# Kernel tuning notes

Measured on AMD Instinct MI355X. Metric: run time of the kernel, lower is better.

Reference implementation:

```python
import jax, jax.numpy as jnp
import numpy as np

NEG_POS_RATIO = 3

def hard_negative_mining(bg_loss, labels, neg_pos_ratio):
    # bg_loss: [B, P] = -log_softmax(conf)[..., 0]; labels: [B, P] int
    pos_mask = labels > 0                               # [B, P]
    num_pos = jnp.sum(pos_mask, axis=1, keepdims=True)  # [B, 1]
    num_neg = num_pos * neg_pos_ratio                   # [B, 1]
    # positives are excluded from the negative ranking
    masked = jnp.where(pos_mask, -jnp.inf, bg_loss)
    # rank of each prior when sorted by loss descending (0 = hardest negative)
    order = jnp.argsort(jnp.argsort(-masked, axis=1), axis=1)
    neg_mask = order < num_neg
    return pos_mask | neg_mask

def setup_inputs() -> dict:
    key = jax.random.key(0)
    k1, k2, k3, k4, k5 = jax.random.split(key, 5)
    B, P, C = 64, 8732, 81
    pred_loc = jax.random.normal(k1, (B, P, 4), dtype=jnp.float32)
    pred_conf = jax.random.normal(k2, (B, P, C), dtype=jnp.float32)
    gt_loc = jax.random.normal(k3, (B, P, 4), dtype=jnp.float32)
    raw_labels = jax.random.randint(k4, (B, P), 0, C)
    is_pos = jax.random.uniform(k5, (B, P)) < 0.02
    gt_labels = jnp.where(is_pos, raw_labels, 0).astype(jnp.int32)
    return {"pred_loc": pred_loc, "pred_conf": pred_conf, "gt_loc": gt_loc, "gt_labels": gt_labels}

def reference(pred_loc, pred_conf, gt_loc, gt_labels):
    # SSD MultiBox loss (training-mode forward of MultiBoxHeads)
    logp = jax.nn.log_softmax(pred_conf, axis=-1)           # [B, P, C]
    bg_loss = -logp[..., 0]                                 # [B, P]
    mask = jax.lax.stop_gradient(
        hard_negative_mining(jax.lax.stop_gradient(bg_loss), gt_labels, NEG_POS_RATIO))
    # cross-entropy with gt labels, summed over kept (pos + hard-neg) priors
    ce = -jnp.take_along_axis(logp, gt_labels[..., None].astype(jnp.int32), axis=-1)[..., 0]
    objectness_loss = jnp.sum(jnp.where(mask, ce, 0.0))
    # smooth L1 on positive priors only
    pos_mask = gt_labels > 0                                # [B, P]
    diff = pred_loc - gt_loc
    absd = jnp.abs(diff)
    sl1 = jnp.where(absd < 1.0, 0.5 * diff * diff, absd - 0.5)
    smooth_l1_loss = jnp.sum(jnp.where(pos_mask[..., None], sl1, 0.0))
    num_pos = jnp.maximum(jnp.sum(pos_mask), 1).astype(jnp.float32)
    return (objectness_loss / num_pos, smooth_l1_loss / num_pos)
```

## Files before the change

kernel.cpp:

```cpp
#include <hip/hip_runtime.h>
#include <cstdint>
#include <cstddef>

#define BATCH 64
#define PRI   8732
#define NCLS  81
#define NEGPOS 3
#define NTOT  (BATCH * PRI)
#define PPB   32
#define NWIN  (NTOT / PPB)
#define WFLOATS (PPB * NCLS)
#define WF4   (WFLOATS / 4)
#define NPERS 1792

__device__ __forceinline__ unsigned keymap(float f) {
    unsigned u = __float_as_uint(f);
    return (u & 0x80000000u) ? ~u : (u | 0x80000000u);
}

__device__ __forceinline__ void gl_lds16(const float4* g, float4* l) {
    __builtin_amdgcn_global_load_lds(
        (const __attribute__((address_space(1))) void*)(const void*)g,
        (__attribute__((address_space(3))) void*)(void*)l, 16, 0, 0);
}

__global__ __launch_bounds__(256) void k_lse(const float* __restrict__ conf,
                                             const int* __restrict__ labels,
                                             const float* __restrict__ ploc,
                                             const float* __restrict__ gloc,
                                             unsigned* __restrict__ keysg,
                                             float* __restrict__ cepart,
                                             float* __restrict__ slpart) {
    __shared__ float lds[2][WFLOATS];
    __shared__ int   labs[2][PPB];
    __shared__ float red0[4], red1[4];
    const int t = threadIdx.x;
    const int bid = blockIdx.x;

    float ceacc = 0.0f, slacc = 0.0f;

    auto stage = [&](int buf, int w) {
        const float4* g4 = reinterpret_cast<const float4*>(conf) + (size_t)w * WF4;
        float4* l4 = reinterpret_cast<float4*>(&lds[buf][0]);
        gl_lds16(&g4[t], &l4[t]);
        gl_lds16(&g4[t + 256], &l4[t + 256]);
        if (t < WF4 - 512) gl_lds16(&g4[t + 512], &l4[t + 512]);
        if (t < PPB) labs[buf][t] = labels[w * PPB + t];
    };

    stage(0, bid);
    __syncthreads();

    int cur = 0;
    for (int i = 0; ; ++i) {
        const int w  = bid + i * NPERS;
        const int wn = w + NPERS;
        const bool more = (wn < NWIN);
        if (more) stage(cur ^ 1, wn);

        const float* ldsw = &lds[cur][0];
        const int q   = t >> 3, h = t & 7;
        const int f0  = q * NCLS + 10 * h;
        const int len = (h == 7) ? 11 : 10;
        const int a0  = f0 & ~3;
        const int o   = f0 & 3;
        const int ve  = o + len;

        const float4* lp = reinterpret_cast<const float4*>(ldsw + a0);
        float4 v0 = lp[0], v1 = lp[1], v2 = lp[2], v3 = lp[3];
        v0.x = (o > 0) ? -INFINITY : v0.x;
        v0.y = (o > 1) ? -INFINITY : v0.y;
        v0.z = (o > 2) ? -INFINITY : v0.z;
        v2.z = (ve > 10) ? v2.z : -INFINITY;
        v2.w = (ve > 11) ? v2.w : -INFINITY;
        v3.x = (ve > 12) ? v3.x : -INFINITY;
        v3.y = (ve > 13) ? v3.y : -INFINITY;
        v3.z = -INFINITY;
        v3.w = -INFINITY;

        float m;
        {
            float a = fmaxf(fmaxf(v0.x, v0.y), fmaxf(v0.z, v0.w));
            float c = fmaxf(fmaxf(v1.x, v1.y), fmaxf(v1.z, v1.w));
            float d = fmaxf(fmaxf(v2.x, v2.y), fmaxf(v2.z, v2.w));
            float e = fmaxf(v3.x, v3.y);
            m = fmaxf(fmaxf(a, c), fmaxf(d, e));
        }
        float s =
            __expf(v0.x - m) + __expf(v0.y - m) + __expf(v0.z - m) + __expf(v0.w - m) +
            __expf(v1.x - m) + __expf(v1.y - m) + __expf(v1.z - m) + __expf(v1.w - m) +
            __expf(v2.x - m) + __expf(v2.y - m) + __expf(v2.z - m) + __expf(v2.w - m) +
            __expf(v3.x - m) + __expf(v3.y - m);

#pragma unroll
        for (int off = 1; off <= 4; off <<= 1) {
            const float mo = __shfl_xor(m, off, 64);
            const float so = __shfl_xor(s, off, 64);
            const float mn = fmaxf(m, mo);
            s = s * __expf(m - mn) + so * __expf(mo - mn);
            m = mn;
        }
        const float lse = m + __logf(s);

        if (h == 0) {
            const int p   = w * PPB + q;
            const int lab = labs[cur][q];
            const float c0 = ldsw[q * NCLS];
            unsigned key = 0u;
            if (lab > 0) {
                ceacc += lse - ldsw[q * NCLS + lab];
                const float4 pl = *reinterpret_cast<const float4*>(ploc + (size_t)p * 4);
                const float4 gl = *reinterpret_cast<const float4*>(gloc + (size_t)p * 4);
                float d, a;
                d = pl.x - gl.x; a = fabsf(d); slacc += (a < 1.0f) ? 0.5f * d * d : a - 0.5f;
                d = pl.y - gl.y; a = fabsf(d); slacc += (a < 1.0f) ? 0.5f * d * d : a - 0.5f;
                d = pl.z - gl.z; a = fabsf(d); slacc += (a < 1.0f) ? 0.5f * d * d : a - 0.5f;
                d = pl.w - gl.w; a = fabsf(d); slacc += (a < 1.0f) ? 0.5f * d * d : a - 0.5f;
            } else {
                key = keymap(lse - c0);
            }
            keysg[p] = key;
        }

        if (!more) break;
        __syncthreads();
        cur ^= 1;
    }

#pragma unroll
    for (int off = 32; off > 0; off >>= 1) {
        ceacc += __shfl_xor(ceacc, off, 64);
        slacc += __shfl_xor(slacc, off, 64);
    }
    const int wid = t >> 6, lane = t & 63;
    __syncthreads();
    if (lane == 0) { red0[wid] = ceacc; red1[wid] = slacc; }
    __syncthreads();
    if (t == 0) {
        cepart[bid] = red0[0] + red0[1] + red0[2] + red0[3];
        slpart[bid] = red1[0] + red1[1] + red1[2] + red1[3];
    }
}

__global__ __launch_bounds__(1024) void k_row(const unsigned* __restrict__ keysg,
                                              float* __restrict__ rowobj,
                                              float* __restrict__ rownp) {
    __shared__ unsigned keys_s[PRI];
    __shared__ unsigned hist[16][257];
    __shared__ unsigned ured[16];
    __shared__ float    fred[16];
    __shared__ unsigned sh_prefix, sh_r;
    __shared__ int      sh_flag;

    const int row  = blockIdx.x;
    const int tid  = threadIdx.x;
    const int wid  = tid >> 6;
    const int lane = tid & 63;
    const unsigned* krow = keysg + (size_t)row * PRI;

    unsigned np = 0;
    for (int j = tid; j < PRI; j += 1024) {
        const unsigned key = krow[j];
        keys_s[j] = key;
        np += (key == 0u) ? 1u : 0u;
    }
#pragma unroll
    for (int off = 32; off > 0; off >>= 1) np += __shfl_xor(np, off, 64);
    if (lane == 0) ured[wid] = np;
    __syncthreads();
    unsigned num_pos = 0;
#pragma unroll
    for (int w = 0; w < 16; ++w) num_pos += ured[w];
    const int k = (int)num_pos * NEGPOS;

    unsigned Kstar = 0xFFFFFFFFu;
    int r_eq = 0;
    bool take_all = false;
    if (k > 0) {
        unsigned prefix = 0;
        int r = k, flag = 0;
        unsigned* hist_flat = &hist[0][0];
        for (int level = 3; level >= 0; --level) {
            const int shift = level * 8;
            for (int i = tid; i < 16 * 257; i += 1024) hist_flat[i] = 0;
            __syncthreads();
            for (int j = tid; j < PRI; j += 1024) {
                const unsigned key = keys_s[j];
                if (key == 0u) continue;
                if (level < 3 && (key >> (shift + 8)) != (prefix >> (shift + 8))) continue;
                atomicAdd(&hist[wid][(key >> shift) & 255u], 1u);
            }
            __syncthreads();
            if (wid == 0) {
                const int b0 = lane * 4;
                unsigned h0 = 0, h1 = 0, h2 = 0, h3 = 0;
#pragma unroll
                for (int w = 0; w < 16; ++w) {
                    h0 += hist[w][b0]; h1 += hist[w][b0 + 1];
                    h2 += hist[w][b0 + 2]; h3 += hist[w][b0 + 3];
                }
                const unsigned loc = h0 + h1 + h2 + h3;
                unsigned ssum = loc;
#pragma unroll
                for (int o2 = 1; o2 < 64; o2 <<= 1) {
                    const unsigned t2 = __shfl_down(ssum, o2, 64);
                    if (lane + o2 < 64) ssum += t2;
                }
                const unsigned above = ssum - loc;
                const unsigned cum3 = above + h3;
                const unsigned cum2 = cum3 + h2;
                const unsigned cum1 = cum2 + h1;
                const unsigned cum0 = cum1 + h0;
                const unsigned long long msk = __ballot(cum0 >= (unsigned)r);
                if (msk == 0ULL) {
                    if (lane == 0) sh_flag = 1;
                } else {
                    const int L = 63 - __clzll(msk);
                    if (lane == L) {
                        unsigned selbin, cumsel, hsel;
                        if      (cum3 >= (unsigned)r) { selbin = b0 + 3; cumsel = cum3; hsel = h3; }
                        else if (cum2 >= (unsigned)r) { selbin = b0 + 2; cumsel = cum2; hsel = h2; }
                        else if (cum1 >= (unsigned)r) { selbin = b0 + 1; cumsel = cum1; hsel = h1; }
                        else                          { selbin = b0;     cumsel = cum0; hsel = h0; }
                        sh_prefix = prefix | (selbin << shift);
                        sh_r = (unsigned)r - (cumsel - hsel);
                        sh_flag = 0;
                    }
                }
            }
            __syncthreads();
            flag = sh_flag;
            if (flag) break;
            prefix = sh_prefix;
            r = (int)sh_r;
        }
        take_all = (flag != 0);
        if (!take_all) { Kstar = prefix; r_eq = r; }
    }

    float obj = 0.0f;
    if (k > 0) {
        for (int j = tid; j < PRI; j += 1024) {
            const unsigned key = keys_s[j];
            if (key != 0u && (take_all || key > Kstar))
                obj += __uint_as_float(key ^ 0x80000000u);
        }
        if (tid == 0 && !take_all)
            obj += (float)r_eq * __uint_as_float(Kstar ^ 0x80000000u);
    }

#pragma unroll
    for (int off = 32; off > 0; off >>= 1) obj += __shfl_xor(obj, off, 64);
    __syncthreads();
    if (lane == 0) fred[wid] = obj;
    __syncthreads();
    if (tid == 0) {
        float to = 0.0f;
#pragma unroll
        for (int w = 0; w < 16; ++w) to += fred[w];
        rowobj[row] = to;
        rownp[row]  = (float)num_pos;
    }
}

__global__ __launch_bounds__(256) void k_final(const float* __restrict__ cepart,
                                               const float* __restrict__ slpart,
                                               const float* __restrict__ rowobj,
                                               const float* __restrict__ rownp,
                                               float* __restrict__ out) {
    const int tid = threadIdx.x;
    float ce = 0.0f, sl = 0.0f;
    for (int i = tid; i < NPERS; i += 256) { ce += cepart[i]; sl += slpart[i]; }
    float ro = 0.0f, np = 0.0f;
    if (tid < BATCH) { ro = rowobj[tid]; np = rownp[tid]; }
#pragma unroll
    for (int off = 32; off > 0; off >>= 1) {
        ce += __shfl_xor(ce, off, 64);
        sl += __shfl_xor(sl, off, 64);
        ro += __shfl_xor(ro, off, 64);
        np += __shfl_xor(np, off, 64);
    }
    __shared__ float r0[4], r1[4], r2[4], r3[4];
    const int wid = tid >> 6, lane = tid & 63;
    if (lane == 0) { r0[wid] = ce; r1[wid] = sl; r2[wid] = ro; r3[wid] = np; }
    __syncthreads();
    if (tid == 0) {
        const float tce = r0[0] + r0[1] + r0[2] + r0[3];
        const float tsl = r1[0] + r1[1] + r1[2] + r1[3];
        const float tro = r2[0] + r2[1] + r2[2] + r2[3];
        const float tnp = r3[0] + r3[1] + r3[2] + r3[3];
        const float npos = fmaxf(tnp, 1.0f);
        out[0] = (tce + tro) / npos;
        out[1] = tsl / npos;
    }
}

extern "C" void kernel_launch(void* const* d_in, const int* in_sizes, int n_in,
                              void* d_out, int out_size, void* d_ws, size_t ws_size,
                              hipStream_t stream) {
    const float* pred_loc  = (const float*)d_in[0];
    const float* pred_conf = (const float*)d_in[1];
    const float* gt_loc    = (const float*)d_in[2];
    const int*   gt_labels = (const int*)d_in[3];
    float* out = (float*)d_out;

    unsigned* keysg   = (unsigned*)d_ws;
    float*    cepart  = (float*)(keysg + NTOT);
    float*    slpart  = cepart + NPERS;
    float*    rowobj  = slpart + NPERS;
    float*    rownp   = rowobj + BATCH;

    k_lse<<<NPERS, 256, 0, stream>>>(pred_conf, gt_labels, pred_loc, gt_loc,
                                     keysg, cepart, slpart);
    k_row<<<BATCH, 1024, 0, stream>>>(keysg, rowobj, rownp);
    k_final<<<1, 256, 0, stream>>>(cepart, slpart, rowobj, rownp, out);
}
```

Measured before the change: 59.35 us.

## Fuse LSE, row selection and final reduction into one persistent kernel

Merges the three kernels into one launch of 256 blocks of 1024 threads. Blocks first compute the log-sum-exp keys over 128-prior windows. The first 64 blocks then spin on a global atomic counter until every block has finished, run the per-row radix selection, and the last row block does the final reduction. This removes two kernel launches and their inter-kernel gaps. In exchange it adds a memset launch, relies on all 256 blocks being co-resident for the grid-wide spin wait, and cuts the number of blocks streaming the large conf tensor.

```diff
diff --git a/kernel.cpp b/kernel.cpp
--- a/kernel.cpp
+++ b/kernel.cpp
@@ -7,11 +7,11 @@
 #define NCLS  81
 #define NEGPOS 3
 #define NTOT  (BATCH * PRI)
-#define PPB   32
+#define PPB   128
 #define NWIN  (NTOT / PPB)
 #define WFLOATS (PPB * NCLS)
 #define WF4   (WFLOATS / 4)
-#define NPERS 1792
+#define NBLKM 256
 
 __device__ __forceinline__ unsigned keymap(float f) {
     unsigned u = __float_as_uint(f);
@@ -24,153 +24,177 @@
         (__attribute__((address_space(3))) void*)(void*)l, 16, 0, 0);
 }
 
-__global__ __launch_bounds__(256) void k_lse(const float* __restrict__ conf,
-                                             const int* __restrict__ labels,
-                                             const float* __restrict__ ploc,
-                                             const float* __restrict__ gloc,
-                                             unsigned* __restrict__ keysg,
-                                             float* __restrict__ cepart,
-                                             float* __restrict__ slpart) {
-    __shared__ float lds[2][WFLOATS];
-    __shared__ int   labs[2][PPB];
-    __shared__ float red0[4], red1[4];
+struct Phase1 {
+    float lds[2][WFLOATS];
+    int   labs[2][PPB];
+    float red0[16], red1[16];
+};
+struct Phase2 {
+    unsigned keys[PRI];
+    unsigned hist[16][257];
+    unsigned ured[16];
+    float    fred[16], fred2[16];
+    unsigned sh_prefix, sh_r;
+    int      sh_flag;
+};
+
+__global__ __launch_bounds__(1024) void k_all(const float* __restrict__ conf,
+                                              const int* __restrict__ labels,
+                                              const float* __restrict__ ploc,
+                                              const float* __restrict__ gloc,
+                                              unsigned* __restrict__ keysg,
+                                              float* __restrict__ cepart,
+                                              float* __restrict__ slpart,
+                                              unsigned* __restrict__ counter,
+                                              float* __restrict__ rowobj,
+                                              float* __restrict__ rownp,
+                                              float* __restrict__ out) {
+    __shared__ union { Phase1 p1; Phase2 p2; } sm;
     const int t = threadIdx.x;
     const int bid = blockIdx.x;
-
-    float ceacc = 0.0f, slacc = 0.0f;
-
-    auto stage = [&](int buf, int w) {
-        const float4* g4 = reinterpret_cast<const float4*>(conf) + (size_t)w * WF4;
-        float4* l4 = reinterpret_cast<float4*>(&lds[buf][0]);
-        gl_lds16(&g4[t], &l4[t]);
-        gl_lds16(&g4[t + 256], &l4[t + 256]);
-        if (t < WF4 - 512) gl_lds16(&g4[t + 512], &l4[t + 512]);
-        if (t < PPB) labs[buf][t] = labels[w * PPB + t];
-    };
-
-    stage(0, bid);
-    __syncthreads();
-
-    int cur = 0;
-    for (int i = 0; ; ++i) {
-        const int w  = bid + i * NPERS;
-        const int wn = w + NPERS;
-        const bool more = (wn < NWIN);
-        if (more) stage(cur ^ 1, wn);
-
-        const float* ldsw = &lds[cur][0];
-        const int q   = t >> 3, h = t & 7;
-        const int f0  = q * NCLS + 10 * h;
-        const int len = (h == 7) ? 11 : 10;
-        const int a0  = f0 & ~3;
-        const int o   = f0 & 3;
-        const int ve  = o + len;
-
-        const float4* lp = reinterpret_cast<const float4*>(ldsw + a0);
-        float4 v0 = lp[0], v1 = lp[1], v2 = lp[2], v3 = lp[3];
-        v0.x = (o > 0) ? -INFINITY : v0.x;
-        v0.y = (o > 1) ? -INFINITY : v0.y;
-        v0.z = (o > 2) ? -INFINITY : v0.z;
-        v2.z = (ve > 10) ? v2.z : -INFINITY;
-        v2.w = (ve > 11) ? v2.w : -INFINITY;
-        v3.x = (ve > 12) ? v3.x : -INFINITY;
-        v3.y = (ve > 13) ? v3.y : -INFINITY;
-        v3.z = -INFINITY;
-        v3.w = -INFINITY;
-
-        float m;
-        {
-            float a = fmaxf(fmaxf(v0.x, v0.y), fmaxf(v0.z, v0.w));
-            float c = fmaxf(fmaxf(v1.x, v1.y), fmaxf(v1.z, v1.w));
-            float d = fmaxf(fmaxf(v2.x, v2.y), fmaxf(v2.z, v2.w));
-            float e = fmaxf(v3.x, v3.y);
-            m = fmaxf(fmaxf(a, c), fmaxf(d, e));
-        }
-        float s =
-            __expf(v0.x - m) + __expf(v0.y - m) + __expf(v0.z - m) + __expf(v0.w - m) +
-            __expf(v1.x - m) + __expf(v1.y - m) + __expf(v1.z - m) + __expf(v1.w - m) +
-            __expf(v2.x - m) + __expf(v2.y - m) + __expf(v2.z - m) + __expf(v2.w - m) +
-            __expf(v3.x - m) + __expf(v3.y - m);
-
-#pragma unroll
-        for (int off = 1; off <= 4; off <<= 1) {
-            const float mo = __shfl_xor(m, off, 64);
-            const float so = __shfl_xor(s, off, 64);
-            const float mn = fmaxf(m, mo);
-            s = s * __expf(m - mn) + so * __expf(mo - mn);
-            m = mn;
-        }
-        const float lse = m + __logf(s);
-
-        if (h == 0) {
-            const int p   = w * PPB + q;
-            const int lab = labs[cur][q];
-            const float c0 = ldsw[q * NCLS];
-            unsigned key = 0u;
-            if (lab > 0) {
-                ceacc += lse - ldsw[q * NCLS + lab];
-                const float4 pl = *reinterpret_cast<const float4*>(ploc + (size_t)p * 4);
-                const float4 gl = *reinterpret_cast<const float4*>(gloc + (size_t)p * 4);
-                float d, a;
-                d = pl.x - gl.x; a = fabsf(d); slacc += (a < 1.0f) ? 0.5f * d * d : a - 0.5f;
-                d = pl.y - gl.y; a = fabsf(d); slacc += (a < 1.0f) ? 0.5f * d * d : a - 0.5f;
-                d = pl.z - gl.z; a = fabsf(d); slacc += (a < 1.0f) ? 0.5f * d * d : a - 0.5f;
-                d = pl.w - gl.w; a = fabsf(d); slacc += (a < 1.0f) ? 0.5f * d * d : a - 0.5f;
-            } else {
-                key = keymap(lse - c0);
-            }
-            keysg[p] = key;
-        }
-
-        if (!more) break;
+    const int wid = t >> 6, lane = t & 63;
+
+    {
+        float ceacc = 0.0f, slacc = 0.0f;
+        const float4* conf4 = reinterpret_cast<const float4*>(conf);
+
+        auto stage = [&](int buf, int w) {
+            const float4* g4 = conf4 + (size_t)w * WF4;
+            float4* l4 = reinterpret_cast<float4*>(&sm.p1.lds[buf][0]);
+            gl_lds16(&g4[t], &l4[t]);
+            gl_lds16(&g4[t + 1024], &l4[t + 1024]);
+            if (t < WF4 - 2048) gl_lds16(&g4[t + 2048], &l4[t + 2048]);
+            if (t < PPB) sm.p1.labs[buf][t] = labels[w * PPB + t];
+        };
+
+        stage(0, bid);
         __syncthreads();
-        cur ^= 1;
-    }
-
-#pragma unroll
-    for (int off = 32; off > 0; off >>= 1) {
-        ceacc += __shfl_xor(ceacc, off, 64);
-        slacc += __shfl_xor(slacc, off, 64);
-    }
-    const int wid = t >> 6, lane = t & 63;
-    __syncthreads();
-    if (lane == 0) { red0[wid] = ceacc; red1[wid] = slacc; }
+
+        int cur = 0;
+        for (int i = 0; ; ++i) {
+            const int w  = bid + i * NBLKM;
+            const int wn = w + NBLKM;
+            const bool more = (wn < NWIN);
+            if (more) stage(cur ^ 1, wn);
+
+            const float* B = &sm.p1.lds[cur][0];
+            const int q   = t >> 3, h = t & 7;
+            const int f0  = q * NCLS + 10 * h;
+            const int len = (h == 7) ? 11 : 10;
+            const int a0  = f0 & ~3;
+            const int o   = f0 & 3;
+            const int ve  = o + len;
+
+            const float4* lp = reinterpret_cast<const float4*>(B + a0);
+            float4 v0 = lp[0], v1 = lp[1], v2 = lp[2], v3 = lp[3];
+            v0.x = (o > 0) ? -INFINITY : v0.x;
+            v0.y = (o > 1) ? -INFINITY : v0.y;
+            v0.z = (o > 2) ? -INFINITY : v0.z;
+            v2.z = (ve > 10) ? v2.z : -INFINITY;
+            v2.w = (ve > 11) ? v2.w : -INFINITY;
+            v3.x = (ve > 12) ? v3.x : -INFINITY;
+            v3.y = (ve > 13) ? v3.y : -INFINITY;
+            v3.z = -INFINITY;
+            v3.w = -INFINITY;
+
+            float m;
+            {
+                float a = fmaxf(fmaxf(v0.x, v0.y), fmaxf(v0.z, v0.w));
+                float c = fmaxf(fmaxf(v1.x, v1.y), fmaxf(v1.z, v1.w));
+                float d = fmaxf(fmaxf(v2.x, v2.y), fmaxf(v2.z, v2.w));
+                float e = fmaxf(v3.x, v3.y);
+                m = fmaxf(fmaxf(a, c), fmaxf(d, e));
+            }
+            float s =
+                __expf(v0.x - m) + __expf(v0.y - m) + __expf(v0.z - m) + __expf(v0.w - m) +
+                __expf(v1.x - m) + __expf(v1.y - m) + __expf(v1.z - m) + __expf(v1.w - m) +
+                __expf(v2.x - m) + __expf(v2.y - m) + __expf(v2.z - m) + __expf(v2.w - m) +
+                __expf(v3.x - m) + __expf(v3.y - m);
+
+#pragma unroll
+            for (int off = 1; off <= 4; off <<= 1) {
+                const float mo = __shfl_xor(m, off, 64);
+                const float so = __shfl_xor(s, off, 64);
+                const float mn = fmaxf(m, mo);
+                s = s * __expf(m - mn) + so * __expf(mo - mn);
+                m = mn;
+            }
+            const float lse = m + __logf(s);
+
+            if (h == 0) {
+                const int p   = w * PPB + q;
+                const int lab = sm.p1.labs[cur][q];
+                const float c0 = B[q * NCLS];
+                unsigned key = 0u;
+                if (lab > 0) {
+                    ceacc += lse - B[q * NCLS + lab];
+                    const float4 pl = *reinterpret_cast<const float4*>(ploc + (size_t)p * 4);
+                    const float4 gl = *reinterpret_cast<const float4*>(gloc + (size_t)p * 4);
+                    float d, a;
+                    d = pl.x - gl.x; a = fabsf(d); slacc += (a < 1.0f) ? 0.5f * d * d : a - 0.5f;
+                    d = pl.y - gl.y; a = fabsf(d); slacc += (a < 1.0f) ? 0.5f * d * d : a - 0.5f;
+                    d = pl.z - gl.z; a = fabsf(d); slacc += (a < 1.0f) ? 0.5f * d * d : a - 0.5f;
+                    d = pl.w - gl.w; a = fabsf(d); slacc += (a < 1.0f) ? 0.5f * d * d : a - 0.5f;
+                } else {
+                    key = keymap(lse - c0);
+                }
+                keysg[p] = key;
+            }
+
+            if (!more) break;
+            __syncthreads();
+            cur ^= 1;
+        }
+
+#pragma unroll
+        for (int off = 32; off > 0; off >>= 1) {
+            ceacc += __shfl_xor(ceacc, off, 64);
+            slacc += __shfl_xor(slacc, off, 64);
+        }
+        __syncthreads();
+        if (lane == 0) { sm.p1.red0[wid] = ceacc; sm.p1.red1[wid] = slacc; }
+        __syncthreads();
+        if (t == 0) {
+            float c2 = 0.0f, s2 = 0.0f;
+#pragma unroll
+            for (int w2 = 0; w2 < 16; ++w2) { c2 += sm.p1.red0[w2]; s2 += sm.p1.red1[w2]; }
+            cepart[bid] = c2;
+            slpart[bid] = s2;
+        }
+    }
+
     __syncthreads();
     if (t == 0) {
-        cepart[bid] = red0[0] + red0[1] + red0[2] + red0[3];
-        slpart[bid] = red1[0] + red1[1] + red1[2] + red1[3];
-    }
-}
-
-__global__ __launch_bounds__(1024) void k_row(const unsigned* __restrict__ keysg,
-                                              float* __restrict__ rowobj,
-                                              float* __restrict__ rownp) {
-    __shared__ unsigned keys_s[PRI];
-    __shared__ unsigned hist[16][257];
-    __shared__ unsigned ured[16];
-    __shared__ float    fred[16];
-    __shared__ unsigned sh_prefix, sh_r;
-    __shared__ int      sh_flag;
-
-    const int row  = blockIdx.x;
-    const int tid  = threadIdx.x;
-    const int wid  = tid >> 6;
-    const int lane = tid & 63;
+        __threadfence();
+        atomicAdd(&counter[0], 1u);
+    }
+    if (bid >= BATCH) return;
+
+    if (t == 0) {
+        while (__hip_atomic_load(&counter[0], __ATOMIC_ACQUIRE,
+                                 __HIP_MEMORY_SCOPE_AGENT) < NBLKM)
+            __builtin_amdgcn_s_sleep(16);
+    }
+    __syncthreads();
+    __threadfence();
+
+    const int row = bid;
     const unsigned* krow = keysg + (size_t)row * PRI;
 
     unsigned np = 0;
-    for (int j = tid; j < PRI; j += 1024) {
+    for (int j = t; j < PRI; j += 1024) {
         const unsigned key = krow[j];
-        keys_s[j] = key;
+        sm.p2.keys[j] = key;
         np += (key == 0u) ? 1u : 0u;
     }
 #pragma unroll
     for (int off = 32; off > 0; off >>= 1) np += __shfl_xor(np, off, 64);
-    if (lane == 0) ured[wid] = np;
+    __syncthreads();
+    if (lane == 0) sm.p2.ured[wid] = np;
     __syncthreads();
     unsigned num_pos = 0;
 #pragma unroll
-    for (int w = 0; w < 16; ++w) num_pos += ured[w];
+    for (int w = 0; w < 16; ++w) num_pos += sm.p2.ured[w];
     const int k = (int)num_pos * NEGPOS;
 
     unsigned Kstar = 0xFFFFFFFFu;
@@ -179,16 +203,16 @@
     if (k > 0) {
         unsigned prefix = 0;
         int r = k, flag = 0;
-        unsigned* hist_flat = &hist[0][0];
+        unsigned* hist_flat = &sm.p2.hist[0][0];
         for (int level = 3; level >= 0; --level) {
             const int shift = level * 8;
-            for (int i = tid; i < 16 * 257; i += 1024) hist_flat[i] = 0;
-            __syncthreads();
-            for (int j = tid; j < PRI; j += 1024) {
-                const unsigned key = keys_s[j];
+            for (int i = t; i < 16 * 257; i += 1024) hist_flat[i] = 0;
+            __syncthreads();
+            for (int j = t; j < PRI; j += 1024) {
+                const unsigned key = sm.p2.keys[j];
                 if (key == 0u) continue;
                 if (level < 3 && (key >> (shift + 8)) != (prefix >> (shift + 8))) continue;
-                atomicAdd(&hist[wid][(key >> shift) & 255u], 1u);
+                atomicAdd(&sm.p2.hist[wid][(key >> shift) & 255u], 1u);
             }
             __syncthreads();
             if (wid == 0) {
@@ -196,8 +220,8 @@
                 unsigned h0 = 0, h1 = 0, h2 = 0, h3 = 0;
 #pragma unroll
                 for (int w = 0; w < 16; ++w) {
-                    h0 += hist[w][b0]; h1 += hist[w][b0 + 1];
-                    h2 += hist[w][b0 + 2]; h3 += hist[w][b0 + 3];
+                    h0 += sm.p2.hist[w][b0];     h1 += sm.p2.hist[w][b0 + 1];
+                    h2 += sm.p2.hist[w][b0 + 2]; h3 += sm.p2.hist[w][b0 + 3];
                 }
                 const unsigned loc = h0 + h1 + h2 + h3;
                 unsigned ssum = loc;
@@ -213,7 +237,7 @@
                 const unsigned cum0 = cum1 + h0;
                 const unsigned long long msk = __ballot(cum0 >= (unsigned)r);
                 if (msk == 0ULL) {
-                    if (lane == 0) sh_flag = 1;
+                    if (lane == 0) sm.p2.sh_flag = 1;
                 } else {
                     const int L = 63 - __clzll(msk);
                     if (lane == L) {
@@ -222,17 +246,18 @@
                         else if (cum2 >= (unsigned)r) { selbin = b0 + 2; cumsel = cum2; hsel = h2; }
                         else if (cum1 >= (unsigned)r) { selbin = b0 + 1; cumsel = cum1; hsel = h1; }
                         else                          { selbin = b0;     cumsel = cum0; hsel = h0; }
-                        sh_prefix = prefix | (selbin << shift);
-                        sh_r = (unsigned)r - (cumsel - hsel);
-                        sh_flag = 0;
+                        sm.p2.sh_prefix = prefix | (selbin << shift);
+                        sm.p2.sh_r = (unsigned)r - (cumsel - hsel);
+                        sm.p2.sh_flag = 0;
                     }
                 }
             }
             __syncthreads();
-            flag = sh_flag;
+            flag = sm.p2.sh_flag;
             if (flag) break;
-            prefix = sh_prefix;
-            r = (int)sh_r;
+            prefix = sm.p2.sh_prefix;
+            r = (int)sm.p2.sh_r;
+            __syncthreads();
         }
         take_all = (flag != 0);
         if (!take_all) { Kstar = prefix; r_eq = r; }
@@ -240,57 +265,61 @@
 
     float obj = 0.0f;
     if (k > 0) {
-        for (int j = tid; j < PRI; j += 1024) {
-            const unsigned key = keys_s[j];
+        for (int j = t; j < PRI; j += 1024) {
+            const unsigned key = sm.p2.keys[j];
             if (key != 0u && (take_all || key > Kstar))
                 obj += __uint_as_float(key ^ 0x80000000u);
         }
-        if (tid == 0 && !take_all)
+        if (t == 0 && !take_all)
             obj += (float)r_eq * __uint_as_float(Kstar ^ 0x80000000u);
     }
 
 #pragma unroll
     for (int off = 32; off > 0; off >>= 1) obj += __shfl_xor(obj, off, 64);
     __syncthreads();
-    if (lane == 0) fred[wid] = obj;
-    __syncthreads();
-    if (tid == 0) {
+    if (lane == 0) sm.p2.fred[wid] = obj;
+    __syncthreads();
+    if (t == 0) {
         float to = 0.0f;
 #pragma unroll
-        for (int w = 0; w < 16; ++w) to += fred[w];
+        for (int w = 0; w < 16; ++w) to += sm.p2.fred[w];
         rowobj[row] = to;
         rownp[row]  = (float)num_pos;
-    }
-}
-
-__global__ __launch_bounds__(256) void k_final(const float* __restrict__ cepart,
-                                               const float* __restrict__ slpart,
-                                               const float* __restrict__ rowobj,
-                                               const float* __restrict__ rownp,
-                                               float* __restrict__ out) {
-    const int tid = threadIdx.x;
-    float ce = 0.0f, sl = 0.0f;
-    for (int i = tid; i < NPERS; i += 256) { ce += cepart[i]; sl += slpart[i]; }
-    float ro = 0.0f, np = 0.0f;
-    if (tid < BATCH) { ro = rowobj[tid]; np = rownp[tid]; }
+        __threadfence();
+        const unsigned t2 = atomicAdd(&counter[1], 1u);
+        sm.p2.sh_flag = (t2 == BATCH - 1) ? -1 : 0;
+    }
+    __syncthreads();
+    if (sm.p2.sh_flag != -1) return;
+
+    __threadfence();
+    float ce = 0.0f, sl = 0.0f, ro = 0.0f, np2 = 0.0f;
+    if (t < NBLKM) { ce = cepart[t]; sl = slpart[t]; }
+    if (t < BATCH) { ro = rowobj[t]; np2 = rownp[t]; }
 #pragma unroll
     for (int off = 32; off > 0; off >>= 1) {
-        ce += __shfl_xor(ce, off, 64);
-        sl += __shfl_xor(sl, off, 64);
-        ro += __shfl_xor(ro, off, 64);
-        np += __shfl_xor(np, off, 64);
-    }
-    __shared__ float r0[4], r1[4], r2[4], r3[4];
-    const int wid = tid >> 6, lane = tid & 63;
-    if (lane == 0) { r0[wid] = ce; r1[wid] = sl; r2[wid] = ro; r3[wid] = np; }
-    __syncthreads();
-    if (tid == 0) {
-        const float tce = r0[0] + r0[1] + r0[2] + r0[3];
-        const float tsl = r1[0] + r1[1] + r1[2] + r1[3];
-        const float tro = r2[0] + r2[1] + r2[2] + r2[3];
-        const float tnp = r3[0] + r3[1] + r3[2] + r3[3];
+        ce  += __shfl_xor(ce,  off, 64);
+        sl  += __shfl_xor(sl,  off, 64);
+        ro  += __shfl_xor(ro,  off, 64);
+        np2 += __shfl_xor(np2, off, 64);
+    }
+    __syncthreads();
+    if (lane == 0) {
+        sm.p2.fred[wid]  = ce + ro;
+        sm.p2.fred2[wid] = sl;
+        sm.p2.ured[wid]  = __float_as_uint(np2);
+    }
+    __syncthreads();
+    if (t == 0) {
+        float tobj = 0.0f, tsl = 0.0f, tnp = 0.0f;
+#pragma unroll
+        for (int w = 0; w < 16; ++w) {
+            tobj += sm.p2.fred[w];
+            tsl  += sm.p2.fred2[w];
+            tnp  += __uint_as_float(sm.p2.ured[w]);
+        }
         const float npos = fmaxf(tnp, 1.0f);
-        out[0] = (tce + tro) / npos;
+        out[0] = tobj / npos;
         out[1] = tsl / npos;
     }
 }
@@ -304,14 +333,15 @@
     const int*   gt_labels = (const int*)d_in[3];
     float* out = (float*)d_out;
 
-    unsigned* keysg   = (unsigned*)d_ws;
+    unsigned* counter = (unsigned*)d_ws;
+    unsigned* keysg   = (unsigned*)d_ws + 4;
     float*    cepart  = (float*)(keysg + NTOT);
-    float*    slpart  = cepart + NPERS;
-    float*    rowobj  = slpart + NPERS;
+    float*    slpart  = cepart + NBLKM;
+    float*    rowobj  = slpart + NBLKM;
     float*    rownp   = rowobj + BATCH;
 
-    k_lse<<<NPERS, 256, 0, stream>>>(pred_conf, gt_labels, pred_loc, gt_loc,
-                                     keysg, cepart, slpart);
-    k_row<<<BATCH, 1024, 0, stream>>>(keysg, rowobj, rownp);
-    k_final<<<1, 256, 0, stream>>>(cepart, slpart, rowobj, rownp, out);
+    hipMemsetAsync(counter, 0, 16, stream);
+    k_all<<<NBLKM, 1024, 0, stream>>>(pred_conf, gt_labels, pred_loc, gt_loc,
+                                      keysg, cepart, slpart, counter,
+                                      rowobj, rownp, out);
 }
```

Result: slower. 97.25 us (+63.9%).
